# Kernel tuning notes

Measured on AMD Instinct MI355X. Metric: run time of the kernel, lower is better.

Reference implementation:

```python
import jax, jax.numpy as jnp
import numpy as np
from jax.scipy.linalg import expm

B, T, N_IN, N_HID, N_OUT = 8192, 2048, 2, 10, 10


def setup_inputs() -> dict:
    key = jax.random.key(0)
    k0, k1, k2, k3, k4 = jax.random.split(key, 5)
    inputs = jax.random.normal(k0, (B, T, N_IN), dtype=jnp.float32)
    # skew-symmetric seed for the orthogonal recurrent kernel (expm parametrization)
    A = jax.random.normal(k1, (N_HID, N_HID), dtype=jnp.float32) * 0.1
    # input_kernel: nn.Linear(n_inputs, n_hidden, bias=False) -> weight [H, D_in]
    W_in = jax.random.normal(k2, (N_HID, N_IN), dtype=jnp.float32) / np.sqrt(N_IN)
    # modrelu bias, initialized uniform(-0.01, 0.01) as in exprnn
    b_mod = jax.random.uniform(k3, (N_HID,), jnp.float32, -0.01, 0.01)
    # final nn.Linear(n_hidden, n_outputs)
    lin_W = jax.random.normal(k4, (N_OUT, N_HID), dtype=jnp.float32) / np.sqrt(N_HID)
    lin_b = jnp.zeros((N_OUT,), jnp.float32)
    return {"inputs": inputs, "A": A, "W_in": W_in, "b_mod": b_mod,
            "lin_W": lin_W, "lin_b": lin_b}


def _modrelu(z, b):
    # modrelu(z) = sign(z) * relu(|z| + b)
    return jnp.sign(z) * jax.nn.relu(jnp.abs(z) + b)


def reference(inputs, A, W_in, b_mod, lin_W, lin_b):
    # Orthogonal recurrent matrix: Bmat = expm(skew(A)), skew from strict upper triangle
    A_tri = jnp.triu(A, k=1)
    Bmat = expm(A_tri - A_tri.T)  # [H, H], orthogonal
    # Precompute input projections for all timesteps: [B, T, H]
    x_proj = jnp.einsum('btd,hd->bth', inputs, W_in)
    h0 = jnp.zeros((inputs.shape[0], W_in.shape[0]), dtype=inputs.dtype)

    def step(h, x_t):
        h_new = _modrelu(x_t + h @ Bmat, b_mod)
        return h_new, None

    hT, _ = jax.lax.scan(step, h0, jnp.swapaxes(x_proj, 0, 1))  # scan over time
    out = hT @ lin_W.T + lin_b  # [B, n_outputs]
    return out
```

## Files before the change

### kernel.cpp

```cpp
#include <hip/hip_runtime.h>

#define H 10
#define T_LEN 2048
#define BATCH 8192

typedef float v2f __attribute__((ext_vector_type(2)));

__device__ __forceinline__ v2f vdup(float s) { v2f r; r.x = s; r.y = s; return r; }
__device__ __forceinline__ v2f vfma2(v2f a, v2f b, v2f c) {
    return __builtin_elementwise_fma(a, b, c);
}

#define ROR2K(x, K) __int_as_float(__builtin_amdgcn_update_dpp(                  \
    0, __float_as_int(x), 0x120 + 2 * (K), 0xF, 0xF, true))

__global__ void expm_kernel(const float* __restrict__ A, float* __restrict__ Bout) {
    __shared__ double S[H][H];
    __shared__ double P[H][H];
    __shared__ double E[H][H];
    const int tid = threadIdx.x;
    const int i = tid / H, j = tid % H;
    if (tid < H * H) {
        double a = 0.0;
        if (i < j) a = (double)A[i * H + j];
        else if (i > j) a = -(double)A[j * H + i];
        a *= (1.0 / 256.0);
        S[i][j] = a;
        P[i][j] = a;
        E[i][j] = (i == j ? 1.0 : 0.0) + a;
    }
    __syncthreads();
    for (int k = 2; k <= 16; ++k) {
        double acc = 0.0;
        if (tid < H * H) {
            for (int m = 0; m < H; ++m) acc += P[i][m] * S[m][j];
            acc *= (1.0 / (double)k);
        }
        __syncthreads();
        if (tid < H * H) { P[i][j] = acc; E[i][j] += acc; }
        __syncthreads();
    }
    for (int rr = 0; rr < 8; ++rr) {
        double acc = 0.0;
        if (tid < H * H) {
            for (int m = 0; m < H; ++m) acc += E[i][m] * E[m][j];
        }
        __syncthreads();
        if (tid < H * H) E[i][j] = acc;
        __syncthreads();
    }
    if (tid < H * H) Bout[i * H + j] = (float)E[i][j];
}

__global__ __launch_bounds__(64)
void rnn_kernel(const float* __restrict__ x,
                const float* __restrict__ Bm,
                const float* __restrict__ Win,
                const float* __restrict__ bmod,
                const float* __restrict__ lW,
                const float* __restrict__ lb,
                float* __restrict__ out) {
    const int lane = threadIdx.x;
    const int l16  = lane & 15;
    const int row  = lane >> 4;
    const int par  = l16 & 1;
    const int q    = l16 >> 1;
    const int bb   = blockIdx.x * 8 + row * 2 + par;
    const int o0   = 2 * q, o1 = o0 + 1;

    v2f Br0[8], Br1[8];
#pragma unroll
    for (int k = 0; k < 8; ++k) {
        const int m = (q - k) & 7;
        const int j0 = 2 * m, j1 = j0 + 1;
        v2f b0 = vdup(0.f), b1 = vdup(0.f);
        if (o0 < H) {
            if (j0 < H) b0.x = Bm[j0 * H + o0];
            if (j1 < H) b1.x = Bm[j1 * H + o0];
        }
        if (o1 < H) {
            if (j0 < H) b0.y = Bm[j0 * H + o1];
            if (j1 < H) b1.y = Bm[j1 * H + o1];
        }
        Br0[k] = b0; Br1[k] = b1;
    }
    v2f w0v = vdup(0.f), w1v = vdup(0.f), bmv = vdup(0.f);
    if (o0 < H) { w0v.x = Win[o0 * 2]; w1v.x = Win[o0 * 2 + 1]; bmv.x = bmod[o0]; }
    if (o1 < H) { w0v.y = Win[o1 * 2]; w1v.y = Win[o1 * 2 + 1]; bmv.y = bmod[o1]; }

    float hx = 0.f, hy = 0.f;

    const float4* __restrict__ xp4 = (const float4*)(x + (size_t)bb * (T_LEN * 2));
    float4 buf[8];
#pragma unroll
    for (int i = 0; i < 8; ++i) buf[i] = xp4[i];

    for (int t0 = 0; t0 < T_LEN; t0 += 16) {
        float4 c[8];
#pragma unroll
        for (int i = 0; i < 8; ++i) c[i] = buf[i];
        if (t0 + 16 < T_LEN) {
            const int base = (t0 + 16) >> 1;
#pragma unroll
            for (int i = 0; i < 8; ++i) buf[i] = xp4[base + i];
        }
        float xs[32];
#pragma unroll
        for (int i = 0; i < 8; ++i) {
            xs[4 * i + 0] = c[i].x; xs[4 * i + 1] = c[i].y;
            xs[4 * i + 2] = c[i].z; xs[4 * i + 3] = c[i].w;
        }

#pragma unroll
        for (int u = 0; u < 16; ++u) {
            const float x0 = xs[2 * u], x1 = xs[2 * u + 1];
            v2f accA = vfma2(vdup(x1), w1v, vdup(x0) * w0v);
            v2f accB = vdup(hx) * Br0[0];
            accA = vfma2(vdup(hy), Br1[0], accA);
#define DOTK(K) { const float ex_ = ROR2K(hx, K); const float ey_ = ROR2K(hy, K); \
                  accB = vfma2(vdup(ex_), Br0[K], accB);                          \
                  accA = vfma2(vdup(ey_), Br1[K], accA); }
            DOTK(1) DOTK(2) DOTK(3) DOTK(4) DOTK(5) DOTK(6) DOTK(7)
#undef DOTK
            const v2f s = accA + accB;
            const float rx = fmaxf(fabsf(s.x) + bmv.x, 0.f);
            const float ry = fmaxf(fabsf(s.y) + bmv.y, 0.f);
            hx = __builtin_copysignf(rx, s.x);
            hy = __builtin_copysignf(ry, s.y);
        }
    }

    v2f L0[8], L1[8];
#pragma unroll
    for (int k = 0; k < 8; ++k) {
        const int m = (q - k) & 7;
        const int j0 = 2 * m, j1 = j0 + 1;
        v2f a0 = vdup(0.f), a1 = vdup(0.f);
        if (o0 < H) {
            if (j0 < H) a0.x = lW[o0 * H + j0];
            if (j1 < H) a1.x = lW[o0 * H + j1];
        }
        if (o1 < H) {
            if (j0 < H) a0.y = lW[o1 * H + j0];
            if (j1 < H) a1.y = lW[o1 * H + j1];
        }
        L0[k] = a0; L1[k] = a1;
    }
    v2f accO = vdup(0.f);
    if (o0 < H) accO.x = lb[o0];
    if (o1 < H) accO.y = lb[o1];
    accO = vfma2(vdup(hx), L0[0], accO);
    accO = vfma2(vdup(hy), L1[0], accO);
#define OUTK(K) { const float ex_ = ROR2K(hx, K); const float ey_ = ROR2K(hy, K); \
                  accO = vfma2(vdup(ex_), L0[K], accO);                           \
                  accO = vfma2(vdup(ey_), L1[K], accO); }
    OUTK(1) OUTK(2) OUTK(3) OUTK(4) OUTK(5) OUTK(6) OUTK(7)
#undef OUTK
    if (o0 < H) {
        float2 st; st.x = accO.x; st.y = accO.y;
        *reinterpret_cast<float2*>(out + (size_t)bb * H + o0) = st;
    }
}

extern "C" void kernel_launch(void* const* d_in, const int* in_sizes, int n_in,
                              void* d_out, int out_size, void* d_ws, size_t ws_size,
                              hipStream_t stream) {
    const float* inputs = (const float*)d_in[0];
    const float* A      = (const float*)d_in[1];
    const float* W_in   = (const float*)d_in[2];
    const float* b_mod  = (const float*)d_in[3];
    const float* lin_W  = (const float*)d_in[4];
    const float* lin_b  = (const float*)d_in[5];
    float* out = (float*)d_out;
    float* Bmat = (float*)d_ws;

    expm_kernel<<<1, 128, 0, stream>>>(A, Bmat);
    rnn_kernel<<<BATCH / 8, 64, 0, stream>>>(inputs, Bmat, W_in, b_mod,
                                             lin_W, lin_b, out);
}
```

Before: 343.2 us.

## Map one hidden unit per lane with 16-lane row rotation instead of packed pairs

Changes the thread-to-work mapping so each lane owns one hidden unit of one batch row, with 4 batch rows per wave instead of 8. The matrix-vector product becomes 16 scalar FMAs with row_ror DPP moves, replacing the 8 packed-FMA steps on two interleaved rows per 16-lane group. The aim is a shorter per-step dependency chain (one accumulator, no final add) at the cost of twice as many waves and less useful work per lane, since 6 of 16 lanes are idle.

```diff
diff --git a/kernel.cpp b/kernel.cpp
--- a/kernel.cpp
+++ b/kernel.cpp
@@ -4,15 +4,8 @@
 #define T_LEN 2048
 #define BATCH 8192
 
-typedef float v2f __attribute__((ext_vector_type(2)));
-
-__device__ __forceinline__ v2f vdup(float s) { v2f r; r.x = s; r.y = s; return r; }
-__device__ __forceinline__ v2f vfma2(v2f a, v2f b, v2f c) {
-    return __builtin_elementwise_fma(a, b, c);
-}
-
-#define ROR2K(x, K) __int_as_float(__builtin_amdgcn_update_dpp(                  \
-    0, __float_as_int(x), 0x120 + 2 * (K), 0xF, 0xF, true))
+#define MOVROR(x, K) __int_as_float(__builtin_amdgcn_mov_dpp(                    \
+    __float_as_int(x), 0x120 + (K), 0xF, 0xF, true))
 
 __global__ void expm_kernel(const float* __restrict__ A, float* __restrict__ Bout) {
     __shared__ double S[H][H];
@@ -61,34 +54,20 @@
                 const float* __restrict__ lb,
                 float* __restrict__ out) {
     const int lane = threadIdx.x;
-    const int l16  = lane & 15;
+    const int j    = lane & 15;
     const int row  = lane >> 4;
-    const int par  = l16 & 1;
-    const int q    = l16 >> 1;
-    const int bb   = blockIdx.x * 8 + row * 2 + par;
-    const int o0   = 2 * q, o1 = o0 + 1;
+    const int bb   = blockIdx.x * 4 + row;
 
-    v2f Br0[8], Br1[8];
+    float Brot[16];
 #pragma unroll
-    for (int k = 0; k < 8; ++k) {
-        const int m = (q - k) & 7;
-        const int j0 = 2 * m, j1 = j0 + 1;
-        v2f b0 = vdup(0.f), b1 = vdup(0.f);
-        if (o0 < H) {
-            if (j0 < H) b0.x = Bm[j0 * H + o0];
-            if (j1 < H) b1.x = Bm[j1 * H + o0];
-        }
-        if (o1 < H) {
-            if (j0 < H) b0.y = Bm[j0 * H + o1];
-            if (j1 < H) b1.y = Bm[j1 * H + o1];
-        }
-        Br0[k] = b0; Br1[k] = b1;
+    for (int k = 0; k < 16; ++k) {
+        const int m = (j - k) & 15;
+        Brot[k] = (j < H && m < H) ? Bm[m * H + j] : 0.f;
     }
-    v2f w0v = vdup(0.f), w1v = vdup(0.f), bmv = vdup(0.f);
-    if (o0 < H) { w0v.x = Win[o0 * 2]; w1v.x = Win[o0 * 2 + 1]; bmv.x = bmod[o0]; }
-    if (o1 < H) { w0v.y = Win[o1 * 2]; w1v.y = Win[o1 * 2 + 1]; bmv.y = bmod[o1]; }
+    float w0j = 0.f, w1j = 0.f, bmj = 0.f;
+    if (j < H) { w0j = Win[j * 2]; w1j = Win[j * 2 + 1]; bmj = bmod[j]; }
 
-    float hx = 0.f, hy = 0.f;
+    float h = 0.f;
 
     const float4* __restrict__ xp4 = (const float4*)(x + (size_t)bb * (T_LEN * 2));
     float4 buf[8];
@@ -104,62 +83,40 @@
 #pragma unroll
             for (int i = 0; i < 8; ++i) buf[i] = xp4[base + i];
         }
-        float xs[32];
-#pragma unroll
-        for (int i = 0; i < 8; ++i) {
-            xs[4 * i + 0] = c[i].x; xs[4 * i + 1] = c[i].y;
-            xs[4 * i + 2] = c[i].z; xs[4 * i + 3] = c[i].w;
-        }
 
 #pragma unroll
         for (int u = 0; u < 16; ++u) {
-            const float x0 = xs[2 * u], x1 = xs[2 * u + 1];
-            v2f accA = vfma2(vdup(x1), w1v, vdup(x0) * w0v);
-            v2f accB = vdup(hx) * Br0[0];
-            accA = vfma2(vdup(hy), Br1[0], accA);
-#define DOTK(K) { const float ex_ = ROR2K(hx, K); const float ey_ = ROR2K(hy, K); \
-                  accB = vfma2(vdup(ex_), Br0[K], accB);                          \
-                  accA = vfma2(vdup(ey_), Br1[K], accA); }
-            DOTK(1) DOTK(2) DOTK(3) DOTK(4) DOTK(5) DOTK(6) DOTK(7)
-#undef DOTK
-            const v2f s = accA + accB;
-            const float rx = fmaxf(fabsf(s.x) + bmv.x, 0.f);
-            const float ry = fmaxf(fabsf(s.y) + bmv.y, 0.f);
-            hx = __builtin_copysignf(rx, s.x);
-            hy = __builtin_copysignf(ry, s.y);
+            const int ii = u >> 1;
+            const float x0 = (u & 1) ? c[ii].z : c[ii].x;
+            const float x1 = (u & 1) ? c[ii].w : c[ii].y;
+
+            float acc = fmaf(x1, w1j, x0 * w0j);
+            acc = fmaf(h, Brot[0], acc);
+#define STEPK(K) { const float e_ = MOVROR(h, K); acc = fmaf(e_, Brot[K], acc); }
+            STEPK(1)  STEPK(2)  STEPK(3)  STEPK(4)  STEPK(5)
+            STEPK(6)  STEPK(7)  STEPK(8)  STEPK(9)  STEPK(10)
+            STEPK(11) STEPK(12) STEPK(13) STEPK(14) STEPK(15)
+#undef STEPK
+            const float s = acc;
+            const float r = fmaxf(fabsf(s) + bmj, 0.f);
+            h = __builtin_copysignf(r, s);
         }
     }
 
-    v2f L0[8], L1[8];
+    float Lrot[16];
 #pragma unroll
-    for (int k = 0; k < 8; ++k) {
-        const int m = (q - k) & 7;
-        const int j0 = 2 * m, j1 = j0 + 1;
-        v2f a0 = vdup(0.f), a1 = vdup(0.f);
-        if (o0 < H) {
-            if (j0 < H) a0.x = lW[o0 * H + j0];
-            if (j1 < H) a1.x = lW[o0 * H + j1];
-        }
-        if (o1 < H) {
-            if (j0 < H) a0.y = lW[o1 * H + j0];
-            if (j1 < H) a1.y = lW[o1 * H + j1];
-        }
-        L0[k] = a0; L1[k] = a1;
+    for (int k = 0; k < 16; ++k) {
+        const int m = (j - k) & 15;
+        Lrot[k] = (j < H && m < H) ? lW[j * H + m] : 0.f;
     }
-    v2f accO = vdup(0.f);
-    if (o0 < H) accO.x = lb[o0];
-    if (o1 < H) accO.y = lb[o1];
-    accO = vfma2(vdup(hx), L0[0], accO);
-    accO = vfma2(vdup(hy), L1[0], accO);
-#define OUTK(K) { const float ex_ = ROR2K(hx, K); const float ey_ = ROR2K(hy, K); \
-                  accO = vfma2(vdup(ex_), L0[K], accO);                           \
-                  accO = vfma2(vdup(ey_), L1[K], accO); }
-    OUTK(1) OUTK(2) OUTK(3) OUTK(4) OUTK(5) OUTK(6) OUTK(7)
+    float acc = (j < H) ? lb[j] : 0.f;
+    acc = fmaf(h, Lrot[0], acc);
+#define OUTK(K) { const float e_ = MOVROR(h, K); acc = fmaf(e_, Lrot[K], acc); }
+    OUTK(1)  OUTK(2)  OUTK(3)  OUTK(4)  OUTK(5)
+    OUTK(6)  OUTK(7)  OUTK(8)  OUTK(9)  OUTK(10)
+    OUTK(11) OUTK(12) OUTK(13) OUTK(14) OUTK(15)
 #undef OUTK
-    if (o0 < H) {
-        float2 st; st.x = accO.x; st.y = accO.y;
-        *reinterpret_cast<float2*>(out + (size_t)bb * H + o0) = st;
-    }
+    if (j < H) out[(size_t)bb * H + j] = acc;
 }
 
 extern "C" void kernel_launch(void* const* d_in, const int* in_sizes, int n_in,
@@ -175,6 +132,6 @@
     float* Bmat = (float*)d_ws;
 
     expm_kernel<<<1, 128, 0, stream>>>(A, Bmat);
-    rnn_kernel<<<BATCH / 8, 64, 0, stream>>>(inputs, Bmat, W_in, b_mod,
+    rnn_kernel<<<BATCH / 4, 64, 0, stream>>>(inputs, Bmat, W_in, b_mod,
                                              lin_W, lin_b, out);
 }
```

New measurement: 389.5 us. 13.5% more time.
